# Kernel tuning notes

Measured on AMD Instinct MI355X. Metric: run time of the kernel, lower is better.

Reference implementation:

```python
import jax, jax.numpy as jnp
import numpy as np

B = 16
D = 512
LENGTHS = [2048 + 256 * i for i in range(B)]  # sum = 63488 tokens (incl. cls per bag)


def _index_maps(lengths):
    # Static (numpy) index maps for ragged <-> padded layout. Each bag's row 0 is a
    # cls token (left untouched); rows 1..L-1 are the conv body.
    lengths = [int(l) for l in np.asarray(lengths).tolist()]
    offs = np.cumsum([0] + lengths)
    lens_b = [l - 1 for l in lengths]            # body lengths after removing cls
    Lmax = max(lens_b)
    Bn = len(lengths)
    pad_src = np.zeros((Bn, Lmax), dtype=np.int32)   # flat x row gathered into [b,t]
    pad_mask = np.zeros((Bn, Lmax), dtype=np.float32)
    body_pos_list, body_b_list, body_t_list = [], [], []
    for i, L in enumerate(lens_b):
        rows = np.arange(offs[i] + 1, offs[i] + 1 + L)
        pad_src[i, :L] = rows
        pad_mask[i, :L] = 1.0
        body_pos_list.append(rows)
        body_b_list.append(np.full(L, i, dtype=np.int32))
        body_t_list.append(np.arange(L, dtype=np.int32))
    body_pos = np.concatenate(body_pos_list)   # flat positions of body tokens
    body_b = np.concatenate(body_b_list)
    body_t = np.concatenate(body_t_list)
    return pad_src, pad_mask, body_pos, body_b, body_t


def _dwconv(xp, w, b):
    # Depthwise 'same' conv1d. xp: [B, D, Lmax], w: [D, 1, k] (torch layout), b: [D].
    y = jax.lax.conv_general_dilated(
        xp, w, window_strides=(1,), padding='SAME',
        feature_group_count=xp.shape[1],
        dimension_numbers=('NCH', 'OIH', 'NCH'))
    return y + b[None, :, None]


def setup_inputs():
    key = jax.random.key(0)
    ks = jax.random.split(key, 7)
    total = sum(LENGTHS)
    x = jax.random.normal(ks[0], (total, D), jnp.float32)
    def u(k, shape, fan):  # torch Conv1d default init: U(-1/sqrt(fan_in*k), ...)
        bound = 1.0 / np.sqrt(fan)
        return jax.random.uniform(k, shape, jnp.float32, -bound, bound)
    w3, b3 = u(ks[1], (D, 1, 3), 3), u(ks[2], (D,), 3)
    w5, b5 = u(ks[3], (D, 1, 5), 5), u(ks[4], (D,), 5)
    w7, b7 = u(ks[5], (D, 1, 7), 7), u(ks[6], (D,), 7)
    lengths = np.array(LENGTHS, dtype=np.int64)
    return {'x': x, 'w3': w3, 'b3': b3, 'w5': w5, 'b5': b5,
            'w7': w7, 'b7': b7, 'lengths': lengths}


def reference(x, w3, b3, w5, b5, w7, b7, lengths):
    pad_src, pad_mask, body_pos, body_b, body_t = _index_maps(lengths)
    # Gather ragged bodies into zero-padded [B, Lmax, D]; zero padding reproduces
    # the per-segment 'same' conv boundary behavior exactly.
    xb = x[pad_src] * pad_mask[:, :, None]
    xp = jnp.transpose(xb, (0, 2, 1))  # [B, D, Lmax]
    y = xp + _dwconv(xp, w3, b3) + _dwconv(xp, w5, b5) + _dwconv(xp, w7, b7)
    body = jnp.transpose(y, (0, 2, 1))[body_b, body_t]  # flat [sum(len-1), D]
    # cls rows keep original x values; body rows replaced by residual conv sum.
    return x.at[body_pos].set(body)
```

## Files before the change

kernel.cpp:

```cpp
#include <hip/hip_runtime.h>

#define DCH 512
#define RPB 16
#define NW  (RPB + 6)

typedef float f32x4 __attribute__((ext_vector_type(4)));

__global__ __launch_bounds__(128) void ppeg_dwconv_kernel(
    const float* __restrict__ x,
    const float* __restrict__ w3, const float* __restrict__ b3,
    const float* __restrict__ w5, const float* __restrict__ b5,
    const float* __restrict__ w7, const float* __restrict__ b7,
    const int* __restrict__ lengths,
    float* __restrict__ out, int n_rows, int n_bags, int nblocks)
{
    __shared__ int soff[40];

    const int tid = threadIdx.x;
    const int c0  = tid * 4;

    int bid = blockIdx.x;
    {
        const int nx = 8;
        const int q  = nblocks / nx, rm = nblocks % nx;
        const int xcd = bid % nx, idx = bid / nx;
        bid = (xcd < rm ? xcd * (q + 1) : rm * (q + 1) + (xcd - rm) * q) + idx;
    }
    const int r0 = bid * RPB;
    if (r0 >= n_rows) return;

    if (tid == 0) {
        int acc = 0;
        for (int i = 0; i < n_bags; ++i) { soff[i] = acc; acc += lengths[i]; }
        soff[n_bags] = acc;
    }

    float W[7][4], bias[4];
    #pragma unroll
    for (int q2 = 0; q2 < 4; ++q2) {
        const int d = c0 + q2;
        const float a0 = w7[d*7+0], a1 = w7[d*7+1], a2 = w7[d*7+2], a3 = w7[d*7+3],
                    a4 = w7[d*7+4], a5 = w7[d*7+5], a6 = w7[d*7+6];
        const float f0 = w5[d*5+0], f1 = w5[d*5+1], f2 = w5[d*5+2], f3 = w5[d*5+3], f4 = w5[d*5+4];
        const float e0 = w3[d*3+0], e1 = w3[d*3+1], e2 = w3[d*3+2];
        W[0][q2] = a0;
        W[1][q2] = a1 + f0;
        W[2][q2] = a2 + f1 + e0;
        W[3][q2] = a3 + f2 + e1 + 1.0f;
        W[4][q2] = a4 + f3 + e2;
        W[5][q2] = a5 + f4;
        W[6][q2] = a6;
        bias[q2] = b3[d] + b5[d] + b7[d];
    }

    __syncthreads();

    int b = 0;
    #pragma unroll
    for (int s = 16; s >= 1; s >>= 1)
        if (b + s < n_bags && soff[b + s] <= r0) b += s;

    const int e0b = soff[b];
    const int e1b = soff[b + 1];
    const int e2b = (b + 2 <= n_bags) ? soff[b + 2] : e1b;

    const bool interior = (r0 >= 3) && (r0 + RPB + 2 < n_rows);

    f32x4 win[NW];
    if (interior) {
        const float* xp = x + (size_t)(r0 - 3) * DCH + c0;
        #pragma unroll
        for (int j = 0; j < NW; ++j) {
            asm volatile("global_load_dwordx4 %0, %1, off"
                         : "=v"(win[j])
                         : "v"(xp + (size_t)j * DCH));
        }
    } else {
        #pragma unroll
        for (int j = 0; j < NW; ++j) {
            const int rr = r0 - 3 + j;
            if (rr >= 0 && rr < n_rows)
                win[j] = *(const f32x4*)(x + (size_t)rr * DCH + c0);
            else
                win[j] = (f32x4){0.f, 0.f, 0.f, 0.f};
        }
    }

    #pragma unroll
    for (int i = 0; i < RPB; ++i) {
        const int r = r0 + i;
        if (r < n_rows) {
            if (interior) {
                asm volatile("s_waitcnt vmcnt(15)" ::: "memory");
                __builtin_amdgcn_sched_barrier(0);
            }

            const bool nb   = (r >= e1b);
            const int  offb = nb ? e1b : e0b;
            const int  endb = nb ? e2b : e1b;
            const int  t    = r - offb - 1;
            const int  Lb1  = endb - offb - 1;

            f32x4 o;
            if (t < 0) {
                o = win[i + 3];
            } else if (t >= 3 && t + 3 < Lb1) {
                float a0 = bias[0], a1 = bias[1], a2 = bias[2], a3 = bias[3];
                #pragma unroll
                for (int dt = 0; dt < 7; ++dt) {
                    const f32x4 v = win[i + dt];
                    a0 = fmaf(W[dt][0], v.x, a0);
                    a1 = fmaf(W[dt][1], v.y, a1);
                    a2 = fmaf(W[dt][2], v.z, a2);
                    a3 = fmaf(W[dt][3], v.w, a3);
                }
                o = (f32x4){a0, a1, a2, a3};
            } else {
                float a0 = bias[0], a1 = bias[1], a2 = bias[2], a3 = bias[3];
                #pragma unroll
                for (int dt = 0; dt < 7; ++dt) {
                    const int  tp    = t + dt - 3;
                    const bool valid = (tp >= 0) && (tp < Lb1);
                    const float mm   = valid ? 1.0f : 0.0f;
                    const f32x4 v = win[i + dt];
                    a0 = fmaf(mm * W[dt][0], v.x, a0);
                    a1 = fmaf(mm * W[dt][1], v.y, a1);
                    a2 = fmaf(mm * W[dt][2], v.z, a2);
                    a3 = fmaf(mm * W[dt][3], v.w, a3);
                }
                o = (f32x4){a0, a1, a2, a3};
            }

            __builtin_nontemporal_store(o, (f32x4*)(out + (size_t)r * DCH + c0));
        }
    }
}

extern "C" void kernel_launch(void* const* d_in, const int* in_sizes, int n_in,
                              void* d_out, int out_size, void* d_ws, size_t ws_size,
                              hipStream_t stream) {
    const float* x       = (const float*)d_in[0];
    const float* w3      = (const float*)d_in[1];
    const float* b3      = (const float*)d_in[2];
    const float* w5      = (const float*)d_in[3];
    const float* b5      = (const float*)d_in[4];
    const float* w7      = (const float*)d_in[5];
    const float* b7      = (const float*)d_in[6];
    const int*   lengths = (const int*)d_in[7];

    const int n_bags = in_sizes[7];
    const int n_rows = in_sizes[0] / DCH;
    float* out = (float*)d_out;

    const int nblocks = (n_rows + RPB - 1) / RPB;
    ppeg_dwconv_kernel<<<nblocks, 128, 0, stream>>>(
        x, w3, b3, w5, b5, w7, b7, lengths, out, n_rows, n_bags, nblocks);
}
```

Measured before the change: 247.2 us.

## Double rows per block and stream halo window with rolling prefetch

Doubles rows per block from 16 to 32, which cuts the redundant 6-row halo reads per block and halves the number of blocks. The interior path now issues the first 13 row loads, then one more load per output row. Each row waits on an explicit vmcnt value computed to cover the issued loads and the outstanding stores. Stores become plain global_store_dwordx4 instead of nontemporal stores. The boundary path is rewritten to load 7 rows per output row. Trade-offs: fewer loads are in flight at the start, fewer blocks lower occupancy, and the hand-computed wait counts must exactly match how the hardware counts loads and stores.

```diff
diff --git a/kernel.cpp b/kernel.cpp
--- a/kernel.cpp
+++ b/kernel.cpp
@@ -1,10 +1,34 @@
 #include <hip/hip_runtime.h>
 
 #define DCH 512
-#define RPB 16
-#define NW  (RPB + 6)
+#define RPB 32
+#define HALO 6
+#define NW  (RPB + HALO)
+#define PFD 6
 
 typedef float f32x4 __attribute__((ext_vector_type(4)));
+
+__device__ __forceinline__ void vmwait_sb(int n) {
+    switch (n) {
+        case 0:  asm volatile("s_waitcnt vmcnt(0)"  ::: "memory"); break;
+        case 1:  asm volatile("s_waitcnt vmcnt(1)"  ::: "memory"); break;
+        case 2:  asm volatile("s_waitcnt vmcnt(2)"  ::: "memory"); break;
+        case 3:  asm volatile("s_waitcnt vmcnt(3)"  ::: "memory"); break;
+        case 4:  asm volatile("s_waitcnt vmcnt(4)"  ::: "memory"); break;
+        case 5:  asm volatile("s_waitcnt vmcnt(5)"  ::: "memory"); break;
+        case 6:  asm volatile("s_waitcnt vmcnt(6)"  ::: "memory"); break;
+        case 7:  asm volatile("s_waitcnt vmcnt(7)"  ::: "memory"); break;
+        case 8:  asm volatile("s_waitcnt vmcnt(8)"  ::: "memory"); break;
+        case 9:  asm volatile("s_waitcnt vmcnt(9)"  ::: "memory"); break;
+        case 10: asm volatile("s_waitcnt vmcnt(10)" ::: "memory"); break;
+        case 11: asm volatile("s_waitcnt vmcnt(11)" ::: "memory"); break;
+        case 12: asm volatile("s_waitcnt vmcnt(12)" ::: "memory"); break;
+        case 13: asm volatile("s_waitcnt vmcnt(13)" ::: "memory"); break;
+        case 14: asm volatile("s_waitcnt vmcnt(14)" ::: "memory"); break;
+        default: asm volatile("s_waitcnt vmcnt(0)"  ::: "memory"); break;
+    }
+    __builtin_amdgcn_sched_barrier(0);
+}
 
 __global__ __launch_bounds__(128) void ppeg_dwconv_kernel(
     const float* __restrict__ x,
@@ -66,40 +90,34 @@
 
     const bool interior = (r0 >= 3) && (r0 + RPB + 2 < n_rows);
 
-    f32x4 win[NW];
     if (interior) {
-        const float* xp = x + (size_t)(r0 - 3) * DCH + c0;
+        const float* xbase = x + (size_t)(r0 - 3) * DCH + c0;
+        float*       obase = out + (size_t)r0 * DCH + c0;
+
+        f32x4 win[NW];
+
         #pragma unroll
-        for (int j = 0; j < NW; ++j) {
+        for (int j = 0; j < 7 + PFD; ++j)
             asm volatile("global_load_dwordx4 %0, %1, off"
-                         : "=v"(win[j])
-                         : "v"(xp + (size_t)j * DCH));
-        }
-    } else {
+                         : "=v"(win[j]) : "v"(xbase + (size_t)j * DCH));
+
         #pragma unroll
-        for (int j = 0; j < NW; ++j) {
-            const int rr = r0 - 3 + j;
-            if (rr >= 0 && rr < n_rows)
-                win[j] = *(const f32x4*)(x + (size_t)rr * DCH + c0);
-            else
-                win[j] = (f32x4){0.f, 0.f, 0.f, 0.f};
-        }
-    }
-
-    #pragma unroll
-    for (int i = 0; i < RPB; ++i) {
-        const int r = r0 + i;
-        if (r < n_rows) {
-            if (interior) {
-                asm volatile("s_waitcnt vmcnt(15)" ::: "memory");
-                __builtin_amdgcn_sched_barrier(0);
-            }
-
-            const bool nb   = (r >= e1b);
-            const int  offb = nb ? e1b : e0b;
-            const int  endb = nb ? e2b : e1b;
-            const int  t    = r - offb - 1;
-            const int  Lb1  = endb - offb - 1;
+        for (int i = 0; i < RPB; ++i) {
+            if (i + 7 + PFD < NW)
+                asm volatile("global_load_dwordx4 %0, %1, off"
+                             : "=v"(win[i + 7 + PFD])
+                             : "v"(xbase + (size_t)(i + 7 + PFD) * DCH));
+
+            const int loads_iss = (i + 7 + PFD < NW) ? (8 + PFD + i) : NW;
+            const int req = (i + 6 <= 6 + PFD) ? (i + 7) : (2 * (i + 6) - 6 - PFD);
+            vmwait_sb(loads_iss + i - req);
+
+            const int r    = r0 + i;
+            const bool nb  = (r >= e1b);
+            const int offb = nb ? e1b : e0b;
+            const int endb = nb ? e2b : e1b;
+            const int t    = r - offb - 1;
+            const int Lb1  = endb - offb - 1;
 
             f32x4 o;
             if (t < 0) {
@@ -131,7 +149,47 @@
                 o = (f32x4){a0, a1, a2, a3};
             }
 
-            __builtin_nontemporal_store(o, (f32x4*)(out + (size_t)r * DCH + c0));
+            asm volatile("global_store_dwordx4 %0, %1, off"
+                         :: "v"(obase + (size_t)i * DCH), "v"(o) : "memory");
+        }
+    } else {
+        for (int i = 0; i < RPB; ++i) {
+            const int r = r0 + i;
+            if (r >= n_rows) break;
+
+            f32x4 wv[7];
+            #pragma unroll
+            for (int dt = 0; dt < 7; ++dt) {
+                const int rr = r - 3 + dt;
+                wv[dt] = (rr >= 0 && rr < n_rows)
+                           ? *(const f32x4*)(x + (size_t)rr * DCH + c0)
+                           : (f32x4){0.f, 0.f, 0.f, 0.f};
+            }
+
+            const bool nb  = (r >= e1b);
+            const int offb = nb ? e1b : e0b;
+            const int endb = nb ? e2b : e1b;
+            const int t    = r - offb - 1;
+            const int Lb1  = endb - offb - 1;
+
+            f32x4 o;
+            if (t < 0) {
+                o = wv[3];
+            } else {
+                float a0 = bias[0], a1 = bias[1], a2 = bias[2], a3 = bias[3];
+                #pragma unroll
+                for (int dt = 0; dt < 7; ++dt) {
+                    const int  tp    = t + dt - 3;
+                    const bool valid = (tp >= 0) && (tp < Lb1);
+                    const float mm   = valid ? 1.0f : 0.0f;
+                    a0 = fmaf(mm * W[dt][0], wv[dt].x, a0);
+                    a1 = fmaf(mm * W[dt][1], wv[dt].y, a1);
+                    a2 = fmaf(mm * W[dt][2], wv[dt].z, a2);
+                    a3 = fmaf(mm * W[dt][3], wv[dt].w, a3);
+                }
+                o = (f32x4){a0, a1, a2, a3};
+            }
+            *(f32x4*)(out + (size_t)r * DCH + c0) = o;
         }
     }
 }
```

Result: slower. 262.1 us (+6.1%).

## Use 256 threads with 2 channels each and a rolling prefetch window

Applied to the files above, without the earlier changes.

Each thread now handles 2 channels instead of 4 and the block has 256 threads. The whole 22-row window is no longer loaded up front: a 13-entry sliding window keeps loads 6 rows ahead and shifts after each output row. The hand-written asm loads and waitcnt are replaced with compiler-scheduled loads. The aim is lower register use and higher occupancy so more memory traffic is in flight, at the cost of narrower 8-byte accesses and reliance on the compiler for load/compute overlap.

```diff
diff --git a/kernel.cpp b/kernel.cpp
--- a/kernel.cpp
+++ b/kernel.cpp
@@ -2,11 +2,12 @@
 
 #define DCH 512
 #define RPB 16
-#define NW  (RPB + 6)
+#define PD  6
+#define WN  (7 + PD)
 
-typedef float f32x4 __attribute__((ext_vector_type(4)));
+typedef float f32x2 __attribute__((ext_vector_type(2)));
 
-__global__ __launch_bounds__(128) void ppeg_dwconv_kernel(
+__global__ __launch_bounds__(256) void ppeg_dwconv_kernel(
     const float* __restrict__ x,
     const float* __restrict__ w3, const float* __restrict__ b3,
     const float* __restrict__ w5, const float* __restrict__ b5,
@@ -17,7 +18,7 @@
     __shared__ int soff[40];
 
     const int tid = threadIdx.x;
-    const int c0  = tid * 4;
+    const int c0  = tid * 2;
 
     int bid = blockIdx.x;
     {
@@ -35,9 +36,9 @@
         soff[n_bags] = acc;
     }
 
-    float W[7][4], bias[4];
+    float W[7][2], bias[2];
     #pragma unroll
-    for (int q2 = 0; q2 < 4; ++q2) {
+    for (int q2 = 0; q2 < 2; ++q2) {
         const int d = c0 + q2;
         const float a0 = w7[d*7+0], a1 = w7[d*7+1], a2 = w7[d*7+2], a3 = w7[d*7+3],
                     a4 = w7[d*7+4], a5 = w7[d*7+5], a6 = w7[d*7+6];
@@ -66,72 +67,94 @@
 
     const bool interior = (r0 >= 3) && (r0 + RPB + 2 < n_rows);
 
-    f32x4 win[NW];
     if (interior) {
-        const float* xp = x + (size_t)(r0 - 3) * DCH + c0;
+        const float* xb = x + (size_t)(r0 - 3) * DCH + c0;
+        float*       ob = out + (size_t)r0 * DCH + c0;
+
+        f32x2 win[WN];
         #pragma unroll
-        for (int j = 0; j < NW; ++j) {
-            asm volatile("global_load_dwordx4 %0, %1, off"
-                         : "=v"(win[j])
-                         : "v"(xp + (size_t)j * DCH));
-        }
-    } else {
+        for (int j = 0; j < WN - 1; ++j)
+            win[j] = *(const f32x2*)(xb + (size_t)j * DCH);
+
         #pragma unroll
-        for (int j = 0; j < NW; ++j) {
-            const int rr = r0 - 3 + j;
-            if (rr >= 0 && rr < n_rows)
-                win[j] = *(const f32x4*)(x + (size_t)rr * DCH + c0);
-            else
-                win[j] = (f32x4){0.f, 0.f, 0.f, 0.f};
-        }
-    }
+        for (int i = 0; i < RPB; ++i) {
+            if (i + PD <= RPB - 1)
+                win[WN - 1] = *(const f32x2*)(xb + (size_t)(i + WN - 1) * DCH);
 
-    #pragma unroll
-    for (int i = 0; i < RPB; ++i) {
-        const int r = r0 + i;
-        if (r < n_rows) {
-            if (interior) {
-                asm volatile("s_waitcnt vmcnt(15)" ::: "memory");
-                __builtin_amdgcn_sched_barrier(0);
-            }
+            const int r    = r0 + i;
+            const bool nb  = (r >= e1b);
+            const int offb = nb ? e1b : e0b;
+            const int endb = nb ? e2b : e1b;
+            const int t    = r - offb - 1;
+            const int Lb1  = endb - offb - 1;
 
-            const bool nb   = (r >= e1b);
-            const int  offb = nb ? e1b : e0b;
-            const int  endb = nb ? e2b : e1b;
-            const int  t    = r - offb - 1;
-            const int  Lb1  = endb - offb - 1;
-
-            f32x4 o;
+            f32x2 o;
             if (t < 0) {
-                o = win[i + 3];
+                o = win[3];
             } else if (t >= 3 && t + 3 < Lb1) {
-                float a0 = bias[0], a1 = bias[1], a2 = bias[2], a3 = bias[3];
+                float a0 = bias[0], a1 = bias[1];
                 #pragma unroll
                 for (int dt = 0; dt < 7; ++dt) {
-                    const f32x4 v = win[i + dt];
+                    const f32x2 v = win[dt];
                     a0 = fmaf(W[dt][0], v.x, a0);
                     a1 = fmaf(W[dt][1], v.y, a1);
-                    a2 = fmaf(W[dt][2], v.z, a2);
-                    a3 = fmaf(W[dt][3], v.w, a3);
                 }
-                o = (f32x4){a0, a1, a2, a3};
+                o = (f32x2){a0, a1};
             } else {
-                float a0 = bias[0], a1 = bias[1], a2 = bias[2], a3 = bias[3];
+                float a0 = bias[0], a1 = bias[1];
                 #pragma unroll
                 for (int dt = 0; dt < 7; ++dt) {
                     const int  tp    = t + dt - 3;
                     const bool valid = (tp >= 0) && (tp < Lb1);
                     const float mm   = valid ? 1.0f : 0.0f;
-                    const f32x4 v = win[i + dt];
+                    const f32x2 v = win[dt];
                     a0 = fmaf(mm * W[dt][0], v.x, a0);
                     a1 = fmaf(mm * W[dt][1], v.y, a1);
-                    a2 = fmaf(mm * W[dt][2], v.z, a2);
-                    a3 = fmaf(mm * W[dt][3], v.w, a3);
                 }
-                o = (f32x4){a0, a1, a2, a3};
+                o = (f32x2){a0, a1};
             }
 
-            __builtin_nontemporal_store(o, (f32x4*)(out + (size_t)r * DCH + c0));
+            __builtin_nontemporal_store(o, (f32x2*)(ob + (size_t)i * DCH));
+
+            #pragma unroll
+            for (int j = 0; j < WN - 1; ++j) win[j] = win[j + 1];
+        }
+    } else {
+        for (int i = 0; i < RPB; ++i) {
+            const int r = r0 + i;
+            if (r >= n_rows) break;
+
+            f32x2 wv[7];
+            #pragma unroll
+            for (int dt = 0; dt < 7; ++dt) {
+                const int rr = r - 3 + dt;
+                wv[dt] = (rr >= 0 && rr < n_rows)
+                           ? *(const f32x2*)(x + (size_t)rr * DCH + c0)
+                           : (f32x2){0.f, 0.f};
+            }
+
+            const bool nb  = (r >= e1b);
+            const int offb = nb ? e1b : e0b;
+            const int endb = nb ? e2b : e1b;
+            const int t    = r - offb - 1;
+            const int Lb1  = endb - offb - 1;
+
+            f32x2 o;
+            if (t < 0) {
+                o = wv[3];
+            } else {
+                float a0 = bias[0], a1 = bias[1];
+                #pragma unroll
+                for (int dt = 0; dt < 7; ++dt) {
+                    const int  tp    = t + dt - 3;
+                    const bool valid = (tp >= 0) && (tp < Lb1);
+                    const float mm   = valid ? 1.0f : 0.0f;
+                    a0 = fmaf(mm * W[dt][0], wv[dt].x, a0);
+                    a1 = fmaf(mm * W[dt][1], wv[dt].y, a1);
+                }
+                o = (f32x2){a0, a1};
+            }
+            *(f32x2*)(out + (size_t)r * DCH + c0) = o;
         }
     }
 }
@@ -153,6 +176,6 @@
     float* out = (float*)d_out;
 
     const int nblocks = (n_rows + RPB - 1) / RPB;
-    ppeg_dwconv_kernel<<<nblocks, 128, 0, stream>>>(
+    ppeg_dwconv_kernel<<<nblocks, 256, 0, stream>>>(
         x, w3, b3, w5, b5, w7, b7, lengths, out, n_rows, n_bags, nblocks);
 }
```

Result: no change. 250.3 us (+1.3%).
